# Optimization experiments

Measured on AMD Instinct MI355X. Metric: run time of the kernel, lower is better.

## Reference

```python
import jax, jax.numpy as jnp
import numpy as np

# E2M1 FP4 value table: codes 0-7 positive, 8-15 negative (sign bit = MSB)
FP4_LUT = jnp.array([0.0, 0.5, 1.0, 1.5, 2.0, 3.0, 4.0, 6.0,
                     -0.0, -0.5, -1.0, -1.5, -2.0, -3.0, -4.0, -6.0],
                    dtype=jnp.float32)
GROUP = 32  # MX microscaling block size


def _dequant(codes, scales):
    # codes: [O, I] int in [0,16); scales: [O, I//GROUP] power-of-two floats
    vals = FP4_LUT[codes]                          # [O, I]
    return vals * jnp.repeat(scales, GROUP, axis=1)  # broadcast group scale


def setup_inputs() -> dict:
    key = jax.random.key(0)
    ks = jax.random.split(key, 7)
    T, D, G = 8192, 4096, GROUP
    x = jax.random.normal(ks[0], (T, D), dtype=jnp.float32)
    w1_codes = jax.random.randint(ks[1], (D, D), 0, 16, dtype=jnp.int32)
    w1_scales = (2.0 ** jax.random.randint(ks[2], (D, D // G), -6, 2)).astype(jnp.float32)
    b1 = jax.random.normal(ks[3], (D,), dtype=jnp.float32) * 0.01
    w2_codes = jax.random.randint(ks[4], (D, D), 0, 16, dtype=jnp.int32)
    w2_scales = (2.0 ** jax.random.randint(ks[5], (D, D // G), -6, 2)).astype(jnp.float32)
    b2 = jax.random.normal(ks[6], (D,), dtype=jnp.float32) * 0.01
    return {"x": x, "w1_codes": w1_codes, "w1_scales": w1_scales, "b1": b1,
            "w2_codes": w2_codes, "w2_scales": w2_scales, "b2": b2}


def reference(x, w1_codes, w1_scales, b1, w2_codes, w2_scales, b2):
    # first MXFP4 quant linear: y = x @ dequant(W1)^T + b1
    h = x @ _dequant(w1_codes, w1_scales).T + b1
    # second MXFP4 quant linear
    y = h @ _dequant(w2_codes, w2_scales).T + b2
    return y
```

## Files before the change

kernel.cpp:

```cpp
#include <hip/hip_runtime.h>


typedef __bf16 bf16;
typedef bf16 bf16x8 __attribute__((ext_vector_type(8)));
typedef float f32x16 __attribute__((ext_vector_type(16)));
typedef int intx4 __attribute__((ext_vector_type(4)));

#define T_DIM 8192
#define D_DIM 4096

__device__ __forceinline__ void gld_lds16(const void* g, void* l) {
    __builtin_amdgcn_global_load_lds(
        (const __attribute__((address_space(1))) void*)g,
        (__attribute__((address_space(3))) void*)l,
        16, 0, 0);
}

__global__ __launch_bounds__(256) void dequant_kernel(
    const int* __restrict__ codes, const float* __restrict__ scales,
    bf16* __restrict__ out)
{
    const size_t tid = (size_t)blockIdx.x * 256 + threadIdx.x;
    const size_t e = tid * 8;
    const int row = (int)(e >> 12);
    const int col = (int)(e & 4095);
    const float s = scales[(size_t)row * (D_DIM / 32) + (col >> 5)];
    const intx4 c0 = *(const intx4*)(codes + e);
    const intx4 c1 = *(const intx4*)(codes + e + 4);
    bf16x8 o;
#pragma unroll
    for (int i = 0; i < 8; ++i) {
        const int c = (i < 4) ? c0[i] : c1[i - 4];
        float v = (float)((0xC8643210u >> ((c & 7) * 4)) & 0xF) * 0.5f;
        v = (c & 8) ? -v : v;
        o[i] = (bf16)(v * s);
    }
    *(bf16x8*)(out + e) = o;
}

__global__ __launch_bounds__(256) void f32_to_bf16_kernel(
    const float* __restrict__ in, bf16* __restrict__ out)
{
    const size_t tid = (size_t)blockIdx.x * 256 + threadIdx.x;
    const size_t e = tid * 8;
    const float4 a = *(const float4*)(in + e);
    const float4 b = *(const float4*)(in + e + 4);
    bf16x8 o;
    o[0] = (bf16)a.x; o[1] = (bf16)a.y; o[2] = (bf16)a.z; o[3] = (bf16)a.w;
    o[4] = (bf16)b.x; o[5] = (bf16)b.y; o[6] = (bf16)b.z; o[7] = (bf16)b.w;
    *(bf16x8*)(out + e) = o;
}

template <bool OUT_BF16>
__global__ __launch_bounds__(256, 2) void gemm_bt_kernel(
    const bf16* __restrict__ A, const bf16* __restrict__ B,
    const float* __restrict__ bias, void* __restrict__ Cout,
    int M, int N, int K)
{
    __shared__ bf16 As[128 * 32];
    __shared__ bf16 Bs[128 * 32];

    const int t = threadIdx.x;
    const int lane = t & 63;
    const int wave = t >> 6;
    const int m0 = blockIdx.y * 128;
    const int n0 = blockIdx.x * 128;
    const int wm = (wave & 1) * 64;
    const int wn = (wave >> 1) * 64;

    f32x16 acc[2][2] = {};

    const int r0 = t >> 2;
    const int c16 = (t & 3) ^ (r0 & 3);
    const int ldsbase = (t & 0xC0) * 16;

    const bf16* pa0 = A + (size_t)(m0 + r0) * K + c16 * 8;
    const bf16* pa1 = A + (size_t)(m0 + r0 + 64) * K + c16 * 8;
    const bf16* pb0 = B + (size_t)(n0 + r0) * K + c16 * 8;
    const bf16* pb1 = B + (size_t)(n0 + r0 + 64) * K + c16 * 8;

    const int rr = lane & 31;
    const int hh = lane >> 5;
    const int sw = lane & 3;

    for (int k0 = 0; k0 < K; k0 += 32) {
        gld_lds16(pa0 + k0, (char*)As + ldsbase);
        gld_lds16(pa1 + k0, (char*)As + 4096 + ldsbase);
        gld_lds16(pb0 + k0, (char*)Bs + ldsbase);
        gld_lds16(pb1 + k0, (char*)Bs + 4096 + ldsbase);
        __syncthreads();

#pragma unroll
        for (int ks = 0; ks < 2; ++ks) {
            const int scol = ((ks * 2 + hh) ^ sw) * 8;
            bf16x8 a[2], b[2];
#pragma unroll
            for (int i = 0; i < 2; ++i) {
                a[i] = *(const bf16x8*)(As + (wm + i * 32 + rr) * 32 + scol);
                b[i] = *(const bf16x8*)(Bs + (wn + i * 32 + rr) * 32 + scol);
            }
#pragma unroll
            for (int i = 0; i < 2; ++i)
#pragma unroll
                for (int j = 0; j < 2; ++j)
                    acc[i][j] = __builtin_amdgcn_mfma_f32_32x32x16_bf16(
                        a[i], b[j], acc[i][j], 0, 0, 0);
        }
        __syncthreads();
    }

    const int cn = lane & 31;
    const int rbase = 4 * hh;
#pragma unroll
    for (int j = 0; j < 2; ++j) {
        const int gn = n0 + wn + j * 32 + cn;
        const float bv = bias[gn];
#pragma unroll
        for (int i = 0; i < 2; ++i) {
#pragma unroll
            for (int reg = 0; reg < 16; ++reg) {
                const int row = (reg & 3) + 8 * (reg >> 2) + rbase;
                const float v = acc[i][j][reg] + bv;
                const size_t idx = (size_t)(m0 + wm + i * 32 + row) * N + gn;
                if (OUT_BF16) ((bf16*)Cout)[idx] = (bf16)v;
                else          ((float*)Cout)[idx] = v;
            }
        }
    }
}

extern "C" void kernel_launch(void* const* d_in, const int* in_sizes, int n_in,
                              void* d_out, int out_size, void* d_ws, size_t ws_size,
                              hipStream_t stream)
{
    const float* x         = (const float*)d_in[0];
    const int*   w1_codes  = (const int*)d_in[1];
    const float* w1_scales = (const float*)d_in[2];
    const float* b1        = (const float*)d_in[3];
    const int*   w2_codes  = (const int*)d_in[4];
    const float* w2_scales = (const float*)d_in[5];
    const float* b2        = (const float*)d_in[6];
    float* y = (float*)d_out;

    char* ws = (char*)d_ws;
    bf16* Xb = (bf16*)ws;
    bf16* Hb = (bf16*)(ws + (size_t)T_DIM * D_DIM * 2);
    bf16* Wd = (bf16*)(ws + (size_t)2 * T_DIM * D_DIM * 2);

    f32_to_bf16_kernel<<<(T_DIM * (size_t)D_DIM) / 8 / 256, 256, 0, stream>>>(x, Xb);
    dequant_kernel<<<(D_DIM * (size_t)D_DIM) / 8 / 256, 256, 0, stream>>>(w1_codes, w1_scales, Wd);
    dim3 grid(D_DIM / 128, T_DIM / 128);
    gemm_bt_kernel<true><<<grid, 256, 0, stream>>>(Xb, Wd, b1, (void*)Hb,
                                                   T_DIM, D_DIM, D_DIM);
    dequant_kernel<<<(D_DIM * (size_t)D_DIM) / 8 / 256, 256, 0, stream>>>(w2_codes, w2_scales, Wd);
    gemm_bt_kernel<false><<<grid, 256, 0, stream>>>(Hb, Wd, b2, (void*)y,
                                                    T_DIM, D_DIM, D_DIM);
}
```

Measured before the change: 928.7 us.

## Fuse prep conversions into one launch and use chunk-major LDS layout

The activation conversion and both weight dequantizations are merged into one prep kernel when the workspace can hold two dequantized weight buffers. This removes separate launches and lets the second weight dequant run ahead of the first GEMM. The GEMM now stores its tiles in LDS as 16-byte k-chunks laid out chunk-major (chunk*1024 + row*8) instead of row-major with an XOR swizzle. Each lane now loads one 16B chunk per row, so a wave's global loads are strided across rows rather than covering contiguous 64B per row, which risks poorer coalescing. The change also needs extra workspace for the second weight buffer.

Result: slower. 1.395 ms (+50.2%).

```diff
diff --git a/kernel.cpp b/kernel.cpp
--- a/kernel.cpp
+++ b/kernel.cpp
@@ -16,12 +16,10 @@
         16, 0, 0);
 }
 
-__global__ __launch_bounds__(256) void dequant_kernel(
-    const int* __restrict__ codes, const float* __restrict__ scales,
-    bf16* __restrict__ out)
+__device__ __forceinline__ void dequant8(
+    const int* __restrict__ codes, const float* __restrict__ scales, bf16* __restrict__ out,
+    size_t e)
 {
-    const size_t tid = (size_t)blockIdx.x * 256 + threadIdx.x;
-    const size_t e = tid * 8;
     const int row = (int)(e >> 12);
     const int col = (int)(e & 4095);
     const float s = scales[(size_t)row * (D_DIM / 32) + (col >> 5)];
@@ -38,17 +36,41 @@
     *(bf16x8*)(out + e) = o;
 }
 
-__global__ __launch_bounds__(256) void f32_to_bf16_kernel(
-    const float* __restrict__ in, bf16* __restrict__ out)
+__device__ __forceinline__ void cvt8(const float* __restrict__ in, bf16* __restrict__ out,
+                                     size_t e)
 {
-    const size_t tid = (size_t)blockIdx.x * 256 + threadIdx.x;
-    const size_t e = tid * 8;
     const float4 a = *(const float4*)(in + e);
     const float4 b = *(const float4*)(in + e + 4);
     bf16x8 o;
     o[0] = (bf16)a.x; o[1] = (bf16)a.y; o[2] = (bf16)a.z; o[3] = (bf16)a.w;
     o[4] = (bf16)b.x; o[5] = (bf16)b.y; o[6] = (bf16)b.z; o[7] = (bf16)b.w;
     *(bf16x8*)(out + e) = o;
+}
+
+__global__ __launch_bounds__(256) void prep_kernel(
+    const float* __restrict__ x, bf16* __restrict__ Xb,
+    const int* __restrict__ w1c, const float* __restrict__ w1s, bf16* __restrict__ Wd1,
+    const int* __restrict__ w2c, const float* __restrict__ w2s, bf16* __restrict__ Wd2)
+{
+    const int b = blockIdx.x;
+    if (b < 16384) {
+        cvt8(x, Xb, ((size_t)b * 256 + threadIdx.x) * 8);
+    } else if (b < 24576) {
+        dequant8(w1c, w1s, Wd1, ((size_t)(b - 16384) * 256 + threadIdx.x) * 8);
+    } else {
+        dequant8(w2c, w2s, Wd2, ((size_t)(b - 24576) * 256 + threadIdx.x) * 8);
+    }
+}
+
+__global__ __launch_bounds__(256) void dequant_kernel(
+    const int* __restrict__ codes, const float* __restrict__ scales, bf16* __restrict__ out)
+{
+    dequant8(codes, scales, out, ((size_t)blockIdx.x * 256 + threadIdx.x) * 8);
+}
+__global__ __launch_bounds__(256) void f32_to_bf16_kernel(
+    const float* __restrict__ in, bf16* __restrict__ out)
+{
+    cvt8(in, out, ((size_t)blockIdx.x * 256 + threadIdx.x) * 8);
 }
 
 template <bool OUT_BF16>
@@ -70,18 +92,17 @@
 
     f32x16 acc[2][2] = {};
 
-    const int r0 = t >> 2;
-    const int c16 = (t & 3) ^ (r0 & 3);
+    const int row = t & 127;
+    const int c0 = t >> 7;
     const int ldsbase = (t & 0xC0) * 16;
 
-    const bf16* pa0 = A + (size_t)(m0 + r0) * K + c16 * 8;
-    const bf16* pa1 = A + (size_t)(m0 + r0 + 64) * K + c16 * 8;
-    const bf16* pb0 = B + (size_t)(n0 + r0) * K + c16 * 8;
-    const bf16* pb1 = B + (size_t)(n0 + r0 + 64) * K + c16 * 8;
+    const bf16* pa0 = A + (size_t)(m0 + row) * K + c0 * 8;
+    const bf16* pa1 = A + (size_t)(m0 + row) * K + (c0 + 2) * 8;
+    const bf16* pb0 = B + (size_t)(n0 + row) * K + c0 * 8;
+    const bf16* pb1 = B + (size_t)(n0 + row) * K + (c0 + 2) * 8;
 
     const int rr = lane & 31;
     const int hh = lane >> 5;
-    const int sw = lane & 3;
 
     for (int k0 = 0; k0 < K; k0 += 32) {
         gld_lds16(pa0 + k0, (char*)As + ldsbase);
@@ -92,12 +113,12 @@
 
 #pragma unroll
         for (int ks = 0; ks < 2; ++ks) {
-            const int scol = ((ks * 2 + hh) ^ sw) * 8;
+            const int c16 = ks * 2 + hh;
             bf16x8 a[2], b[2];
 #pragma unroll
             for (int i = 0; i < 2; ++i) {
-                a[i] = *(const bf16x8*)(As + (wm + i * 32 + rr) * 32 + scol);
-                b[i] = *(const bf16x8*)(Bs + (wn + i * 32 + rr) * 32 + scol);
+                a[i] = *(const bf16x8*)(As + c16 * 1024 + (wm + i * 32 + rr) * 8);
+                b[i] = *(const bf16x8*)(Bs + c16 * 1024 + (wn + i * 32 + rr) * 8);
             }
 #pragma unroll
             for (int i = 0; i < 2; ++i)
@@ -119,9 +140,9 @@
         for (int i = 0; i < 2; ++i) {
 #pragma unroll
             for (int reg = 0; reg < 16; ++reg) {
-                const int row = (reg & 3) + 8 * (reg >> 2) + rbase;
+                const int orow = (reg & 3) + 8 * (reg >> 2) + rbase;
                 const float v = acc[i][j][reg] + bv;
-                const size_t idx = (size_t)(m0 + wm + i * 32 + row) * N + gn;
+                const size_t idx = (size_t)(m0 + wm + i * 32 + orow) * N + gn;
                 if (OUT_BF16) ((bf16*)Cout)[idx] = (bf16)v;
                 else          ((float*)Cout)[idx] = v;
             }
@@ -143,16 +164,30 @@
     float* y = (float*)d_out;
 
     char* ws = (char*)d_ws;
-    bf16* Xb = (bf16*)ws;
-    bf16* Hb = (bf16*)(ws + (size_t)T_DIM * D_DIM * 2);
-    bf16* Wd = (bf16*)(ws + (size_t)2 * T_DIM * D_DIM * 2);
+    const size_t XB = (size_t)T_DIM * D_DIM * 2;
+    const size_t WB = (size_t)D_DIM * D_DIM * 2;
+    bf16* Xb  = (bf16*)ws;
+    bf16* Hb  = (bf16*)(ws + XB);
+    bf16* Wd1 = (bf16*)(ws + 2 * XB);
+    dim3 grid(D_DIM / 128, T_DIM / 128);
 
-    f32_to_bf16_kernel<<<(T_DIM * (size_t)D_DIM) / 8 / 256, 256, 0, stream>>>(x, Xb);
-    dequant_kernel<<<(D_DIM * (size_t)D_DIM) / 8 / 256, 256, 0, stream>>>(w1_codes, w1_scales, Wd);
-    dim3 grid(D_DIM / 128, T_DIM / 128);
-    gemm_bt_kernel<true><<<grid, 256, 0, stream>>>(Xb, Wd, b1, (void*)Hb,
-                                                   T_DIM, D_DIM, D_DIM);
-    dequant_kernel<<<(D_DIM * (size_t)D_DIM) / 8 / 256, 256, 0, stream>>>(w2_codes, w2_scales, Wd);
-    gemm_bt_kernel<false><<<grid, 256, 0, stream>>>(Hb, Wd, b2, (void*)y,
-                                                    T_DIM, D_DIM, D_DIM);
+    if (ws_size >= 2 * XB + 2 * WB) {
+        bf16* Wd2 = (bf16*)(ws + 2 * XB + WB);
+        prep_kernel<<<32768, 256, 0, stream>>>(x, Xb, w1_codes, w1_scales, Wd1,
+                                               w2_codes, w2_scales, Wd2);
+        gemm_bt_kernel<true><<<grid, 256, 0, stream>>>(Xb, Wd1, b1, (void*)Hb,
+                                                       T_DIM, D_DIM, D_DIM);
+        gemm_bt_kernel<false><<<grid, 256, 0, stream>>>(Hb, Wd2, b2, (void*)y,
+                                                        T_DIM, D_DIM, D_DIM);
+    } else {
+        f32_to_bf16_kernel<<<(T_DIM * (size_t)D_DIM) / 8 / 256, 256, 0, stream>>>(x, Xb);
+        dequant_kernel<<<(D_DIM * (size_t)D_DIM) / 8 / 256, 256, 0, stream>>>(
+            w1_codes, w1_scales, Wd1);
+        gemm_bt_kernel<true><<<grid, 256, 0, stream>>>(Xb, Wd1, b1, (void*)Hb,
+                                                       T_DIM, D_DIM, D_DIM);
+        dequant_kernel<<<(D_DIM * (size_t)D_DIM) / 8 / 256, 256, 0, stream>>>(
+            w2_codes, w2_scales, Wd1);
+        gemm_bt_kernel<false><<<grid, 256, 0, stream>>>(Hb, Wd1, b2, (void*)y,
+                                                        T_DIM, D_DIM, D_DIM);
+    }
 }
```
